# Kernel optimization log

Hardware: AMD Instinct MI355X
Metric: run time of the kernel (lower is better)

## Reference

```python
import jax, jax.numpy as jnp
import numpy as np

B, N, D = 8, 2048, 512  # batch, input_dim (tokens), weight_dim


def setup_inputs() -> dict:
    key = jax.random.key(0)
    ks = jax.random.split(key, 7)
    return {
        "query": jax.random.normal(ks[0], (B, N, D), dtype=jnp.float32),
        "key": jax.random.normal(ks[1], (B, N, D), dtype=jnp.float32),
        "value": jax.random.normal(ks[2], (B, N, D), dtype=jnp.float32),
        "W_query": jax.random.normal(ks[3], (D, D), dtype=jnp.float32),
        "W_key": jax.random.normal(ks[4], (D, D), dtype=jnp.float32),
        "W_value": jax.random.normal(ks[5], (D, D), dtype=jnp.float32),
        "self_importance": jnp.zeros((N,), dtype=jnp.float32),
    }


def reference(query, key, value, W_query, W_key, W_value, self_importance):
    d = W_query.shape[0]
    q = jnp.einsum("bnd,de->bne", query, W_query)
    k = jnp.einsum("bnd,de->bne", key, W_key)
    v = jnp.einsum("bnd,de->bne", value, W_value)
    scores = jnp.einsum("bqe,bke->bqk", q, k) / jnp.sqrt(jnp.float32(d))
    # diagonal self-importance bias: eye(N) * clamp(exp(s), max=3)
    importance = jnp.minimum(jnp.exp(self_importance), 3.0)  # [N]
    n = scores.shape[1]
    idx = jnp.arange(n)
    scores = scores.at[:, idx, idx].add(importance)
    attn = jax.nn.softmax(scores, axis=-1)  # [B, N, N]
    entropy_loss = -jnp.mean(jnp.sum(attn * jnp.log(attn + 1e-10), axis=-1))
    out = jnp.einsum("bqk,bke->bqe", attn, v)
    return (out, attn, entropy_loss)
```

## Files before the change

### kernel.cpp

```cpp
#include <hip/hip_runtime.h>
#include <math.h>

#define BB 8
#define NN 2048
#define DD 512

typedef _Float16 halfT;
typedef _Float16 half8 __attribute__((ext_vector_type(8)));
typedef _Float16 half4 __attribute__((ext_vector_type(4)));
typedef float f32x4 __attribute__((ext_vector_type(4)));

#define GLOAD16(gp, sp) __builtin_amdgcn_global_load_lds( \
    (const __attribute__((address_space(1))) void*)(gp), \
    (__attribute__((address_space(3))) void*)(sp), 16, 0, 0)

__global__ __launch_bounds__(256) void wsplit_kernel(
    const float* __restrict__ Wq, const float* __restrict__ Wk, const float* __restrict__ Wv,
    _Float16* __restrict__ qhT, _Float16* __restrict__ qlT,
    _Float16* __restrict__ khT, _Float16* __restrict__ klT,
    _Float16* __restrict__ vhT)
{
    __shared__ float t[64][65];
    const int z = blockIdx.z;
    const float* W = (z == 0) ? Wq : ((z == 1) ? Wk : Wv);
    _Float16* Ph = (z == 0) ? qhT : ((z == 1) ? khT : vhT);
    _Float16* Pl = (z == 0) ? qlT : ((z == 1) ? klT : nullptr);
    const int bx = blockIdx.x * 64, by = blockIdx.y * 64;
    const int tid = threadIdx.x;
    #pragma unroll
    for (int i = 0; i < 16; ++i) {
        const int idx = i * 256 + tid;
        const int r = idx >> 6, c = idx & 63;
        t[r][c] = W[(long)(by + r) * 512 + bx + c];
    }
    __syncthreads();
    #pragma unroll
    for (int i = 0; i < 16; ++i) {
        const int idx = i * 256 + tid;
        const int r = idx >> 6, c = idx & 63;
        const float v = t[c][r];
        const _Float16 h = (_Float16)v;
        const long o = (long)(bx + r) * 512 + by + c;
        Ph[o] = h;
        if (z < 2) Pl[o] = (_Float16)(v - (float)h);
    }
}

__global__ __launch_bounds__(256) void projqk_kernel(
    const float* __restrict__ Af0, const float* __restrict__ Af1,
    const _Float16* __restrict__ B0h, const _Float16* __restrict__ B0l,
    const _Float16* __restrict__ B1h, const _Float16* __restrict__ B1l,
    _Float16* __restrict__ O0h, _Float16* __restrict__ O0l,
    _Float16* __restrict__ O1h, _Float16* __restrict__ O1l)
{
    __shared__ __align__(16) _Float16 smem[4 * 128 * 32];
    _Float16* Ah = smem;
    _Float16* Bh = smem + 4096;
    _Float16* Al = smem + 8192;
    _Float16* Bl = smem + 12288;

    const int z = blockIdx.z;
    const float* Af = z ? Af1 : Af0;
    const _Float16* Bgh = z ? B1h : B0h;
    const _Float16* Bgl = z ? B1l : B0l;
    _Float16* Oh = z ? O1h : O0h;
    _Float16* Ol = z ? O1l : O0l;

    const int tid  = threadIdx.x;
    const int lane = tid & 63;
    const int w    = tid >> 6;
    const int wr   = w >> 1, wc = w & 1;
    const int bm   = blockIdx.y * 128, bn = blockIdx.x * 128;

    f32x4 acc[4][4];
    #pragma unroll
    for (int i = 0; i < 4; ++i)
        #pragma unroll
        for (int j = 0; j < 4; ++j) acc[i][j] = (f32x4)0.0f;

    for (int k0 = 0; k0 < DD; k0 += 32) {
        #pragma unroll
        for (int i = 0; i < 2; ++i) {
            const int c   = i * 256 + w * 64 + lane;
            const int row = c >> 2, sl = c & 3;
            const long g  = (long)(bn + row) * DD + k0 + sl * 8;
            const int lb  = (i * 256 + w * 64) * 8;
            GLOAD16(Bgh + g, Bh + lb);
            GLOAD16(Bgl + g, Bl + lb);
        }
        #pragma unroll
        for (int i = 0; i < 4; ++i) {
            const int c = tid + i * 256;
            const int row = c >> 3, q4 = c & 7;
            const float4 v = *(const float4*)(Af + (long)(bm + row) * DD + k0 + q4 * 4);
            half4 h;
            h[0] = (_Float16)v.x; h[1] = (_Float16)v.y;
            h[2] = (_Float16)v.z; h[3] = (_Float16)v.w;
            *(half4*)&Ah[row * 32 + q4 * 4] = h;
            half4 l;
            l[0] = (_Float16)(v.x - (float)h[0]);
            l[1] = (_Float16)(v.y - (float)h[1]);
            l[2] = (_Float16)(v.z - (float)h[2]);
            l[3] = (_Float16)(v.w - (float)h[3]);
            *(half4*)&Al[row * 32 + q4 * 4] = l;
        }
        __syncthreads();

        half8 ah[4], bh[4], al[4], bl[4];
        #pragma unroll
        for (int f = 0; f < 4; ++f) {
            const int ar = wr * 64 + f * 16 + (lane & 15);
            const int ao = ar * 32 + ((lane >> 4) << 3);
            ah[f] = *(const half8*)&Ah[ao];
            al[f] = *(const half8*)&Al[ao];
            const int br = wc * 64 + f * 16 + (lane & 15);
            const int bo = br * 32 + ((lane >> 4) << 3);
            bh[f] = *(const half8*)&Bh[bo];
            bl[f] = *(const half8*)&Bl[bo];
        }
        #pragma unroll
        for (int i = 0; i < 4; ++i)
            #pragma unroll
            for (int j = 0; j < 4; ++j) {
                acc[i][j] = __builtin_amdgcn_mfma_f32_16x16x32_f16(ah[i], bh[j], acc[i][j], 0, 0, 0);
                acc[i][j] = __builtin_amdgcn_mfma_f32_16x16x32_f16(ah[i], bl[j], acc[i][j], 0, 0, 0);
                acc[i][j] = __builtin_amdgcn_mfma_f32_16x16x32_f16(al[i], bh[j], acc[i][j], 0, 0, 0);
            }
        __syncthreads();
    }

    #pragma unroll
    for (int i = 0; i < 4; ++i) {
        const int rb = bm + wr * 64 + i * 16 + ((lane >> 4) << 2);
        #pragma unroll
        for (int j = 0; j < 4; ++j) {
            const int gc = bn + wc * 64 + j * 16 + (lane & 15);
            #pragma unroll
            for (int r = 0; r < 4; ++r) {
                const float vv = acc[i][j][r];
                const _Float16 h = (_Float16)vv;
                const long o = (long)(rb + r) * DD + gc;
                Oh[o] = h;
                Ol[o] = (_Float16)(vv - (float)h);
            }
        }
    }
}

template<int EPI>
__global__ __launch_bounds__(256) void mm_nt(
    const float* __restrict__ Af,
    const _Float16* __restrict__ Agh,
    const _Float16* __restrict__ Bgh,
    float* __restrict__ Of, _Float16* __restrict__ Oh,
    int N, int K, long sAb, long sBb, long sOb)
{
    constexpr bool A_FP32 = (EPI == 1);

    __shared__ __align__(16) _Float16 smem[2 * 128 * 32];
    _Float16* Ah = smem;
    _Float16* Bh = smem + 4096;

    const int tid  = threadIdx.x;
    const int lane = tid & 63;
    const int w    = tid >> 6;
    const int wr   = w >> 1, wc = w & 1;
    const int z    = blockIdx.z;
    const int bm   = blockIdx.y * 128, bn = blockIdx.x * 128;

    const float* Afz = nullptr;
    const _Float16* Aghz = nullptr;
    if constexpr (A_FP32) { Afz = Af + (long)z * sAb; }
    else { Aghz = Agh + (long)z * sAb; }
    const _Float16* Bghz = Bgh + (long)z * sBb;

    f32x4 acc[4][4];
    #pragma unroll
    for (int i = 0; i < 4; ++i)
        #pragma unroll
        for (int j = 0; j < 4; ++j) acc[i][j] = (f32x4)0.0f;

    for (int k0 = 0; k0 < K; k0 += 32) {
        #pragma unroll
        for (int i = 0; i < 2; ++i) {
            const int c   = i * 256 + w * 64 + lane;
            const int row = c >> 2, sl = c & 3;
            const long g  = (long)(bn + row) * K + k0 + sl * 8;
            const int lb  = (i * 256 + w * 64) * 8;
            GLOAD16(Bghz + g, Bh + lb);
        }
        if constexpr (A_FP32) {
            #pragma unroll
            for (int i = 0; i < 4; ++i) {
                const int c = tid + i * 256;
                const int row = c >> 3, q4 = c & 7;
                const float4 v = *(const float4*)(Afz + (long)(bm + row) * K + k0 + q4 * 4);
                half4 h;
                h[0] = (_Float16)v.x; h[1] = (_Float16)v.y;
                h[2] = (_Float16)v.z; h[3] = (_Float16)v.w;
                *(half4*)&Ah[row * 32 + q4 * 4] = h;
            }
        } else {
            #pragma unroll
            for (int i = 0; i < 2; ++i) {
                const int c   = i * 256 + w * 64 + lane;
                const int row = c >> 2, sl = c & 3;
                const long g  = (long)(bm + row) * K + k0 + sl * 8;
                const int lb  = (i * 256 + w * 64) * 8;
                GLOAD16(Aghz + g, Ah + lb);
            }
        }
        __syncthreads();

        half8 ah[4], bh[4];
        #pragma unroll
        for (int f = 0; f < 4; ++f) {
            const int ar = wr * 64 + f * 16 + (lane & 15);
            const int ao = ar * 32 + ((lane >> 4) << 3);
            ah[f] = *(const half8*)&Ah[ao];
            const int br = wc * 64 + f * 16 + (lane & 15);
            const int bo = br * 32 + ((lane >> 4) << 3);
            bh[f] = *(const half8*)&Bh[bo];
        }
        #pragma unroll
        for (int i = 0; i < 4; ++i)
            #pragma unroll
            for (int j = 0; j < 4; ++j)
                acc[i][j] = __builtin_amdgcn_mfma_f32_16x16x32_f16(ah[i], bh[j], acc[i][j], 0, 0, 0);
        __syncthreads();
    }

    #pragma unroll
    for (int i = 0; i < 4; ++i) {
        const int rb = bm + wr * 64 + i * 16 + ((lane >> 4) << 2);
        #pragma unroll
        for (int j = 0; j < 4; ++j) {
            const int gc = bn + wc * 64 + j * 16 + (lane & 15);
            if constexpr (EPI == 1) {
                half4 hv;
                #pragma unroll
                for (int r = 0; r < 4; ++r) hv[r] = (_Float16)acc[i][j][r];
                const int b = rb >> 11, rIn = rb & 2047;
                *(half4*)&Oh[((long)b * 512 + gc) * 2048 + rIn] = hv;
            } else {
                float* O = Of + (long)z * sOb;
                #pragma unroll
                for (int r = 0; r < 4; ++r)
                    O[(long)(rb + r) * N + gc] = acc[i][j][r];
            }
        }
    }
}

__global__ __launch_bounds__(512, 2) void scores256_kernel(
    const halfT* __restrict__ qh, const halfT* __restrict__ ql,
    const halfT* __restrict__ kh, const halfT* __restrict__ kl,
    float* __restrict__ C, const float* __restrict__ si, float scale)
{
    extern __shared__ __align__(16) char smem[];

    const int tid  = threadIdx.x;
    const int lane = tid & 63;
    const int w    = tid >> 6;
    const int wr   = w >> 2, wc = w & 3;

    int flat = (blockIdx.z << 6) | (blockIdx.y << 3) | blockIdx.x;
    flat = ((flat & 7) << 6) | (flat >> 3);
    const int bx = flat & 7, by = (flat >> 3) & 7, bz = flat >> 6;
    const int bm = by * 256, bn = bx * 256;

    const long zoff = (long)bz * NN * DD;
    const halfT* A_h = qh + zoff;
    const halfT* A_l = ql + zoff;
    const halfT* B_h = kh + zoff;
    const halfT* B_l = kl + zoff;

    const int s_row   = w * 16 + (lane >> 2);
    const int s_chunk = (lane & 3) ^ ((lane >> 3) & 3);
    const long gA = (long)(bm + s_row) * DD + s_chunk * 8;
    const long gB = (long)(bn + s_row) * DD + s_chunk * 8;
    const int ldst = w * 1024;
    const long rstep = (long)128 * DD;

    const int lr   = lane & 15;
    const int q16  = lane >> 4;
    const int frag = lr * 64 + ((q16 ^ ((lr >> 1) & 3)) << 4);
    const int abase = wr * 8192 + frag;
    const int bbase = wc * 4096 + frag;

    f32x4 acc[8][4];
    #pragma unroll
    for (int m = 0; m < 8; ++m)
        #pragma unroll
        for (int n = 0; n < 4; ++n) acc[m][n] = (f32x4)0.0f;

    {
        char* b0 = smem;
        GLOAD16(A_h + gA,         b0 + ldst);
        GLOAD16(A_h + gA + rstep, b0 + 8192 + ldst);
        GLOAD16(A_l + gA,         b0 + 16384 + ldst);
        GLOAD16(A_l + gA + rstep, b0 + 16384 + 8192 + ldst);
        GLOAD16(B_h + gB,         b0 + 32768 + ldst);
        GLOAD16(B_h + gB + rstep, b0 + 32768 + 8192 + ldst);
        GLOAD16(B_l + gB,         b0 + 49152 + ldst);
        GLOAD16(B_l + gB + rstep, b0 + 49152 + 8192 + ldst);
    }
    asm volatile("s_waitcnt vmcnt(0)" ::: "memory");
    __builtin_amdgcn_s_barrier();
    __builtin_amdgcn_sched_barrier(0);

    for (int t = 0; t < 16; ++t) {
        char* cur = smem + (size_t)(t & 1) * 65536;
        char* nxt = smem + (size_t)((t + 1) & 1) * 65536;
        const bool pf = (t < 15);
        const long kk = (long)(t + 1) * 32;

        half8 ah[8], bh[4];
        #pragma unroll
        for (int n = 0; n < 4; ++n)
            bh[n] = *(const half8*)(cur + 32768 + bbase + n * 1024);
        #pragma unroll
        for (int m = 0; m < 8; ++m)
            ah[m] = *(const half8*)(cur + abase + m * 1024);
        if (pf) {
            GLOAD16(A_h + gA + kk,         nxt + ldst);
            GLOAD16(A_h + gA + rstep + kk, nxt + 8192 + ldst);
            GLOAD16(A_l + gA + kk,         nxt + 16384 + ldst);
            GLOAD16(A_l + gA + rstep + kk, nxt + 16384 + 8192 + ldst);
        }
        __builtin_amdgcn_s_barrier();
        asm volatile("s_waitcnt lgkmcnt(0)" ::: "memory");
        __builtin_amdgcn_sched_barrier(0);
        __builtin_amdgcn_s_setprio(1);
        #pragma unroll
        for (int m = 0; m < 8; ++m)
            #pragma unroll
            for (int n = 0; n < 4; ++n)
                acc[m][n] = __builtin_amdgcn_mfma_f32_16x16x32_f16(ah[m], bh[n], acc[m][n], 0, 0, 0);
        __builtin_amdgcn_s_setprio(0);
        __builtin_amdgcn_s_barrier();
        __builtin_amdgcn_sched_barrier(0);

        half8 bl[4];
        #pragma unroll
        for (int n = 0; n < 4; ++n)
            bl[n] = *(const half8*)(cur + 49152 + bbase + n * 1024);
        if (pf) {
            GLOAD16(B_h + gB + kk,         nxt + 32768 + ldst);
            GLOAD16(B_h + gB + rstep + kk, nxt + 32768 + 8192 + ldst);
            GLOAD16(B_l + gB + kk,         nxt + 49152 + ldst);
            GLOAD16(B_l + gB + rstep + kk, nxt + 49152 + 8192 + ldst);
        }
        __builtin_amdgcn_s_barrier();
        asm volatile("s_waitcnt lgkmcnt(0)" ::: "memory");
        __builtin_amdgcn_sched_barrier(0);
        __builtin_amdgcn_s_setprio(1);
        #pragma unroll
        for (int m = 0; m < 8; ++m)
            #pragma unroll
            for (int n = 0; n < 4; ++n)
                acc[m][n] = __builtin_amdgcn_mfma_f32_16x16x32_f16(ah[m], bl[n], acc[m][n], 0, 0, 0);
        __builtin_amdgcn_s_setprio(0);
        __builtin_amdgcn_s_barrier();
        __builtin_amdgcn_sched_barrier(0);

        half8 al[8];
        #pragma unroll
        for (int m = 0; m < 8; ++m)
            al[m] = *(const half8*)(cur + 16384 + abase + m * 1024);
        __builtin_amdgcn_s_barrier();
        asm volatile("s_waitcnt lgkmcnt(0)" ::: "memory");
        __builtin_amdgcn_sched_barrier(0);
        __builtin_amdgcn_s_setprio(1);
        #pragma unroll
        for (int m = 0; m < 8; ++m)
            #pragma unroll
            for (int n = 0; n < 4; ++n)
                acc[m][n] = __builtin_amdgcn_mfma_f32_16x16x32_f16(al[m], bh[n], acc[m][n], 0, 0, 0);
        __builtin_amdgcn_s_setprio(0);
        if (pf) { asm volatile("s_waitcnt vmcnt(0)" ::: "memory"); }
        __builtin_amdgcn_s_barrier();
        __builtin_amdgcn_sched_barrier(0);
    }

    float* Cz = C + (long)bz * NN * NN;
    #pragma unroll
    for (int m = 0; m < 8; ++m) {
        const int rb = bm + wr * 128 + m * 16 + ((lane >> 4) << 2);
        #pragma unroll
        for (int n = 0; n < 4; ++n) {
            const int gc = bn + wc * 64 + n * 16 + (lane & 15);
            #pragma unroll
            for (int r = 0; r < 4; ++r) {
                const int gr = rb + r;
                float vv = acc[m][n][r] * scale;
                if (gr == gc) vv += fminf(expf(si[gr]), 3.0f);
                Cz[(long)gr * NN + gc] = vv;
            }
        }
    }
}

__global__ __launch_bounds__(256) void softmax_entropy_kernel(
    float* __restrict__ attn, _Float16* __restrict__ ah, float* __restrict__ partials)
{
    __shared__ float red[4];
    const long row = blockIdx.x;
    float* p = attn + row * (long)NN;
    _Float16* ph = ah + row * (long)NN;
    const int tid = threadIdx.x;
    const int base = tid * 8;

    float4 va = *(const float4*)(p + base);
    float4 vb = *(const float4*)(p + base + 4);
    float v[8] = {va.x, va.y, va.z, va.w, vb.x, vb.y, vb.z, vb.w};

    float m = v[0];
    #pragma unroll
    for (int i = 1; i < 8; ++i) m = fmaxf(m, v[i]);
    #pragma unroll
    for (int o = 32; o; o >>= 1) m = fmaxf(m, __shfl_xor(m, o, 64));
    if ((tid & 63) == 0) red[tid >> 6] = m;
    __syncthreads();
    m = fmaxf(fmaxf(red[0], red[1]), fmaxf(red[2], red[3]));

    float t[8];
    float s = 0.f;
    #pragma unroll
    for (int i = 0; i < 8; ++i) { t[i] = v[i] - m; v[i] = expf(t[i]); s += v[i]; }
    #pragma unroll
    for (int o = 32; o; o >>= 1) s += __shfl_xor(s, o, 64);
    __syncthreads();
    if ((tid & 63) == 0) red[tid >> 6] = s;
    __syncthreads();
    s = red[0] + red[1] + red[2] + red[3];

    const float inv = 1.0f / s;
    const float lns = logf(s);
    float e = 0.f;
    float pv[8];
    #pragma unroll
    for (int i = 0; i < 8; ++i) {
        pv[i] = v[i] * inv;
        e = fmaf(pv[i], t[i] - lns, e);
    }
    *(float4*)(p + base)     = make_float4(pv[0], pv[1], pv[2], pv[3]);
    *(float4*)(p + base + 4) = make_float4(pv[4], pv[5], pv[6], pv[7]);
    half8 h;
    #pragma unroll
    for (int i = 0; i < 8; ++i) h[i] = (_Float16)pv[i];
    *(half8*)(ph + base) = h;

    #pragma unroll
    for (int o = 32; o; o >>= 1) e += __shfl_xor(e, o, 64);
    __syncthreads();
    if ((tid & 63) == 0) red[tid >> 6] = e;
    __syncthreads();
    if (tid == 0) partials[row] = red[0] + red[1] + red[2] + red[3];
}

__global__ __launch_bounds__(256) void ent_reduce_kernel(
    const float* __restrict__ partials, float* __restrict__ ent)
{
    __shared__ float red[4];
    float s = 0.f;
    for (int i = threadIdx.x; i < BB * NN; i += 256) s += partials[i];
    #pragma unroll
    for (int o = 32; o; o >>= 1) s += __shfl_xor(s, o, 64);
    if ((threadIdx.x & 63) == 0) red[threadIdx.x >> 6] = s;
    __syncthreads();
    if (threadIdx.x == 0)
        *ent = -(red[0] + red[1] + red[2] + red[3]) / (float)(BB * NN);
}

extern "C" void kernel_launch(void* const* d_in, const int* in_sizes, int n_in,
                              void* d_out, int out_size, void* d_ws, size_t ws_size,
                              hipStream_t stream) {
    const float* query = (const float*)d_in[0];
    const float* key   = (const float*)d_in[1];
    const float* value = (const float*)d_in[2];
    const float* Wq    = (const float*)d_in[3];
    const float* Wk    = (const float*)d_in[4];
    const float* Wv    = (const float*)d_in[5];
    const float* si    = (const float*)d_in[6];

    float* out  = (float*)d_out;
    float* attn = out + (size_t)BB * NN * DD;
    float* ent  = attn + (size_t)BB * NN * NN;

    const size_t NK = (size_t)BB * NN * DD;
    _Float16* ws16 = (_Float16*)d_ws;
    _Float16* qh = ws16;
    _Float16* ql = qh + NK;
    _Float16* kh = ql + NK;
    _Float16* kl = kh + NK;
    _Float16* vT = kl + NK;
    _Float16* WqhT = vT + NK;
    _Float16* WqlT = WqhT + DD * DD;
    _Float16* WkhT = WqlT + DD * DD;
    _Float16* WklT = WkhT + DD * DD;
    _Float16* WvhT = WklT + DD * DD;
    float* partials = (float*)(WvhT + DD * DD);
    _Float16* attn_h = ws16;

    const dim3 blk(256);
    const float inv_sqrt_d = 0.044194173824159216f;

    wsplit_kernel<<<dim3(8, 8, 3), blk, 0, stream>>>(Wq, Wk, Wv,
        WqhT, WqlT, WkhT, WklT, WvhT);

    projqk_kernel<<<dim3(4, 128, 2), blk, 0, stream>>>(
        query, key, WqhT, WqlT, WkhT, WklT, qh, ql, kh, kl);
    mm_nt<1><<<dim3(4, 128, 1), blk, 0, stream>>>(
        value, nullptr, WvhT, nullptr, vT, DD, DD, 0, 0, 0);

    scores256_kernel<<<dim3(8, 8, 8), dim3(512), 131072, stream>>>(
        qh, ql, kh, kl, attn, si, inv_sqrt_d);

    softmax_entropy_kernel<<<dim3(BB * NN), blk, 0, stream>>>(attn, attn_h, partials);
    ent_reduce_kernel<<<dim3(1), blk, 0, stream>>>(partials, ent);

    mm_nt<3><<<dim3(4, 16, BB), blk, 0, stream>>>(
        nullptr, attn_h, vT, out, nullptr, DD, NN,
        (long)NN * NN, (long)DD * NN, (long)NN * DD);
}
```

Before: 335.7 us.

## Switch scores GEMM to 32x32 MFMA and add pipelined attn-V kernel

The scores kernel now uses 32x32x16 f16 MFMA tiles, which cuts LDS fragment reads per FLOP. It also issues the whole next-stage prefetch up front and drops the intermediate barriers, keeping one wait-and-barrier per k-step. The attn·V product moves from the generic 128x128 mm_nt to a new 256x128, 512-thread kernel with double-buffered LDS, direct-to-LDS loads, swizzled fragments and 32x32 MFMA. The V projection becomes a dedicated non-template kernel. The gain is higher MFMA throughput and better overlap. The costs are higher register pressure from the 16-wide accumulators and less fine-grained interleaving of loads with compute.

Result: no change. 335.0 us (-0.2%).

```diff
diff --git a/kernel.cpp b/kernel.cpp
--- a/kernel.cpp
+++ b/kernel.cpp
@@ -9,6 +9,7 @@
 typedef _Float16 half8 __attribute__((ext_vector_type(8)));
 typedef _Float16 half4 __attribute__((ext_vector_type(4)));
 typedef float f32x4 __attribute__((ext_vector_type(4)));
+typedef float f32x16 __attribute__((ext_vector_type(16)));
 
 #define GLOAD16(gp, sp) __builtin_amdgcn_global_load_lds( \
     (const __attribute__((address_space(1))) void*)(gp), \
@@ -147,16 +148,10 @@
     }
 }
 
-template<int EPI>
-__global__ __launch_bounds__(256) void mm_nt(
-    const float* __restrict__ Af,
-    const _Float16* __restrict__ Agh,
-    const _Float16* __restrict__ Bgh,
-    float* __restrict__ Of, _Float16* __restrict__ Oh,
-    int N, int K, long sAb, long sBb, long sOb)
-{
-    constexpr bool A_FP32 = (EPI == 1);
-
+__global__ __launch_bounds__(256) void vproj_kernel(
+    const float* __restrict__ Af, const _Float16* __restrict__ Bgh,
+    _Float16* __restrict__ Oh)
+{
     __shared__ __align__(16) _Float16 smem[2 * 128 * 32];
     _Float16* Ah = smem;
     _Float16* Bh = smem + 4096;
@@ -165,50 +160,32 @@
     const int lane = tid & 63;
     const int w    = tid >> 6;
     const int wr   = w >> 1, wc = w & 1;
-    const int z    = blockIdx.z;
     const int bm   = blockIdx.y * 128, bn = blockIdx.x * 128;
 
-    const float* Afz = nullptr;
-    const _Float16* Aghz = nullptr;
-    if constexpr (A_FP32) { Afz = Af + (long)z * sAb; }
-    else { Aghz = Agh + (long)z * sAb; }
-    const _Float16* Bghz = Bgh + (long)z * sBb;
-
     f32x4 acc[4][4];
     #pragma unroll
     for (int i = 0; i < 4; ++i)
         #pragma unroll
         for (int j = 0; j < 4; ++j) acc[i][j] = (f32x4)0.0f;
 
-    for (int k0 = 0; k0 < K; k0 += 32) {
+    for (int k0 = 0; k0 < DD; k0 += 32) {
         #pragma unroll
         for (int i = 0; i < 2; ++i) {
             const int c   = i * 256 + w * 64 + lane;
             const int row = c >> 2, sl = c & 3;
-            const long g  = (long)(bn + row) * K + k0 + sl * 8;
+            const long g  = (long)(bn + row) * DD + k0 + sl * 8;
             const int lb  = (i * 256 + w * 64) * 8;
-            GLOAD16(Bghz + g, Bh + lb);
-        }
-        if constexpr (A_FP32) {
-            #pragma unroll
-            for (int i = 0; i < 4; ++i) {
-                const int c = tid + i * 256;
-                const int row = c >> 3, q4 = c & 7;
-                const float4 v = *(const float4*)(Afz + (long)(bm + row) * K + k0 + q4 * 4);
-                half4 h;
-                h[0] = (_Float16)v.x; h[1] = (_Float16)v.y;
-                h[2] = (_Float16)v.z; h[3] = (_Float16)v.w;
-                *(half4*)&Ah[row * 32 + q4 * 4] = h;
-            }
-        } else {
-            #pragma unroll
-            for (int i = 0; i < 2; ++i) {
-                const int c   = i * 256 + w * 64 + lane;
-                const int row = c >> 2, sl = c & 3;
-                const long g  = (long)(bm + row) * K + k0 + sl * 8;
-                const int lb  = (i * 256 + w * 64) * 8;
-                GLOAD16(Aghz + g, Ah + lb);
-            }
+            GLOAD16(Bgh + g, Bh + lb);
+        }
+        #pragma unroll
+        for (int i = 0; i < 4; ++i) {
+            const int c = tid + i * 256;
+            const int row = c >> 3, q4 = c & 7;
+            const float4 v = *(const float4*)(Af + (long)(bm + row) * DD + k0 + q4 * 4);
+            half4 h;
+            h[0] = (_Float16)v.x; h[1] = (_Float16)v.y;
+            h[2] = (_Float16)v.z; h[3] = (_Float16)v.w;
+            *(half4*)&Ah[row * 32 + q4 * 4] = h;
         }
         __syncthreads();
 
@@ -216,11 +193,9 @@
         #pragma unroll
         for (int f = 0; f < 4; ++f) {
             const int ar = wr * 64 + f * 16 + (lane & 15);
-            const int ao = ar * 32 + ((lane >> 4) << 3);
-            ah[f] = *(const half8*)&Ah[ao];
+            ah[f] = *(const half8*)&Ah[ar * 32 + ((lane >> 4) << 3)];
             const int br = wc * 64 + f * 16 + (lane & 15);
-            const int bo = br * 32 + ((lane >> 4) << 3);
-            bh[f] = *(const half8*)&Bh[bo];
+            bh[f] = *(const half8*)&Bh[br * 32 + ((lane >> 4) << 3)];
         }
         #pragma unroll
         for (int i = 0; i < 4; ++i)
@@ -236,18 +211,11 @@
         #pragma unroll
         for (int j = 0; j < 4; ++j) {
             const int gc = bn + wc * 64 + j * 16 + (lane & 15);
-            if constexpr (EPI == 1) {
-                half4 hv;
-                #pragma unroll
-                for (int r = 0; r < 4; ++r) hv[r] = (_Float16)acc[i][j][r];
-                const int b = rb >> 11, rIn = rb & 2047;
-                *(half4*)&Oh[((long)b * 512 + gc) * 2048 + rIn] = hv;
-            } else {
-                float* O = Of + (long)z * sOb;
-                #pragma unroll
-                for (int r = 0; r < 4; ++r)
-                    O[(long)(rb + r) * N + gc] = acc[i][j][r];
-            }
+            half4 hv;
+            #pragma unroll
+            for (int r = 0; r < 4; ++r) hv[r] = (_Float16)acc[i][j][r];
+            const int b = rb >> 11, rIn = rb & 2047;
+            *(half4*)&Oh[((long)b * 512 + gc) * 2048 + rIn] = hv;
         }
     }
 }
@@ -282,29 +250,28 @@
     const int ldst = w * 1024;
     const long rstep = (long)128 * DD;
 
-    const int lr   = lane & 15;
-    const int q16  = lane >> 4;
-    const int frag = lr * 64 + ((q16 ^ ((lr >> 1) & 3)) << 4);
-    const int abase = wr * 8192 + frag;
-    const int bbase = wc * 4096 + frag;
-
-    f32x4 acc[8][4];
-    #pragma unroll
-    for (int m = 0; m < 8; ++m)
-        #pragma unroll
-        for (int n = 0; n < 4; ++n) acc[m][n] = (f32x4)0.0f;
-
-    {
-        char* b0 = smem;
-        GLOAD16(A_h + gA,         b0 + ldst);
-        GLOAD16(A_h + gA + rstep, b0 + 8192 + ldst);
-        GLOAD16(A_l + gA,         b0 + 16384 + ldst);
-        GLOAD16(A_l + gA + rstep, b0 + 16384 + 8192 + ldst);
-        GLOAD16(B_h + gB,         b0 + 32768 + ldst);
-        GLOAD16(B_h + gB + rstep, b0 + 32768 + 8192 + ldst);
-        GLOAD16(B_l + gB,         b0 + 49152 + ldst);
-        GLOAD16(B_l + gB + rstep, b0 + 49152 + 8192 + ldst);
-    }
+    auto stage = [&](char* buf, int t) {
+        const long kk = (long)t * 32;
+        GLOAD16(A_h + gA + kk,         buf + ldst);
+        GLOAD16(A_h + gA + rstep + kk, buf + 8192 + ldst);
+        GLOAD16(A_l + gA + kk,         buf + 16384 + ldst);
+        GLOAD16(A_l + gA + rstep + kk, buf + 16384 + 8192 + ldst);
+        GLOAD16(B_h + gB + kk,         buf + 32768 + ldst);
+        GLOAD16(B_h + gB + rstep + kk, buf + 32768 + 8192 + ldst);
+        GLOAD16(B_l + gB + kk,         buf + 49152 + ldst);
+        GLOAD16(B_l + gB + rstep + kk, buf + 49152 + 8192 + ldst);
+    };
+
+    const int frow = lane & 31;
+    const int fgr  = lane >> 5;
+
+    f32x16 acc[4][2];
+    #pragma unroll
+    for (int m = 0; m < 4; ++m)
+        #pragma unroll
+        for (int n = 0; n < 2; ++n) acc[m][n] = (f32x16)0.0f;
+
+    stage(smem, 0);
     asm volatile("s_waitcnt vmcnt(0)" ::: "memory");
     __builtin_amdgcn_s_barrier();
     __builtin_amdgcn_sched_barrier(0);
@@ -312,91 +279,176 @@
     for (int t = 0; t < 16; ++t) {
         char* cur = smem + (size_t)(t & 1) * 65536;
         char* nxt = smem + (size_t)((t + 1) & 1) * 65536;
-        const bool pf = (t < 15);
-        const long kk = (long)(t + 1) * 32;
-
-        half8 ah[8], bh[4];
-        #pragma unroll
-        for (int n = 0; n < 4; ++n)
-            bh[n] = *(const half8*)(cur + 32768 + bbase + n * 1024);
-        #pragma unroll
-        for (int m = 0; m < 8; ++m)
-            ah[m] = *(const half8*)(cur + abase + m * 1024);
-        if (pf) {
-            GLOAD16(A_h + gA + kk,         nxt + ldst);
-            GLOAD16(A_h + gA + rstep + kk, nxt + 8192 + ldst);
-            GLOAD16(A_l + gA + kk,         nxt + 16384 + ldst);
-            GLOAD16(A_l + gA + rstep + kk, nxt + 16384 + 8192 + ldst);
-        }
-        __builtin_amdgcn_s_barrier();
-        asm volatile("s_waitcnt lgkmcnt(0)" ::: "memory");
-        __builtin_amdgcn_sched_barrier(0);
+
+        if (t < 15) stage(nxt, t + 1);
+
+        auto fr = [&](const char* unit, int row, int kh) -> half8 {
+            const int g = kh * 2 + fgr;
+            const int phys = g ^ ((row >> 1) & 3);
+            return *(const half8*)(unit + row * 64 + phys * 16);
+        };
+
+        half8 a_[4][2], bh_[2][2];
+        #pragma unroll
+        for (int kh2 = 0; kh2 < 2; ++kh2) {
+            #pragma unroll
+            for (int n = 0; n < 2; ++n)
+                bh_[n][kh2] = fr(cur + 32768, wc * 64 + n * 32 + frow, kh2);
+            #pragma unroll
+            for (int m = 0; m < 4; ++m)
+                a_[m][kh2] = fr(cur, wr * 128 + m * 32 + frow, kh2);
+        }
         __builtin_amdgcn_s_setprio(1);
         #pragma unroll
-        for (int m = 0; m < 8; ++m)
-            #pragma unroll
-            for (int n = 0; n < 4; ++n)
-                acc[m][n] = __builtin_amdgcn_mfma_f32_16x16x32_f16(ah[m], bh[n], acc[m][n], 0, 0, 0);
+        for (int m = 0; m < 4; ++m)
+            #pragma unroll
+            for (int n = 0; n < 2; ++n)
+                #pragma unroll
+                for (int kh2 = 0; kh2 < 2; ++kh2)
+                    acc[m][n] = __builtin_amdgcn_mfma_f32_32x32x16_f16(a_[m][kh2], bh_[n][kh2], acc[m][n], 0, 0, 0);
         __builtin_amdgcn_s_setprio(0);
-        __builtin_amdgcn_s_barrier();
-        __builtin_amdgcn_sched_barrier(0);
-
-        half8 bl[4];
-        #pragma unroll
-        for (int n = 0; n < 4; ++n)
-            bl[n] = *(const half8*)(cur + 49152 + bbase + n * 1024);
-        if (pf) {
-            GLOAD16(B_h + gB + kk,         nxt + 32768 + ldst);
-            GLOAD16(B_h + gB + rstep + kk, nxt + 32768 + 8192 + ldst);
-            GLOAD16(B_l + gB + kk,         nxt + 49152 + ldst);
-            GLOAD16(B_l + gB + rstep + kk, nxt + 49152 + 8192 + ldst);
-        }
-        __builtin_amdgcn_s_barrier();
-        asm volatile("s_waitcnt lgkmcnt(0)" ::: "memory");
-        __builtin_amdgcn_sched_barrier(0);
+
+        half8 bl_[2][2];
+        #pragma unroll
+        for (int kh2 = 0; kh2 < 2; ++kh2)
+            #pragma unroll
+            for (int n = 0; n < 2; ++n)
+                bl_[n][kh2] = fr(cur + 49152, wc * 64 + n * 32 + frow, kh2);
         __builtin_amdgcn_s_setprio(1);
         #pragma unroll
-        for (int m = 0; m < 8; ++m)
-            #pragma unroll
-            for (int n = 0; n < 4; ++n)
-                acc[m][n] = __builtin_amdgcn_mfma_f32_16x16x32_f16(ah[m], bl[n], acc[m][n], 0, 0, 0);
+        for (int m = 0; m < 4; ++m)
+            #pragma unroll
+            for (int n = 0; n < 2; ++n)
+                #pragma unroll
+                for (int kh2 = 0; kh2 < 2; ++kh2)
+                    acc[m][n] = __builtin_amdgcn_mfma_f32_32x32x16_f16(a_[m][kh2], bl_[n][kh2], acc[m][n], 0, 0, 0);
         __builtin_amdgcn_s_setprio(0);
-        __builtin_amdgcn_s_barrier();
-        __builtin_amdgcn_sched_barrier(0);
-
-        half8 al[8];
-        #pragma unroll
-        for (int m = 0; m < 8; ++m)
-            al[m] = *(const half8*)(cur + 16384 + abase + m * 1024);
-        __builtin_amdgcn_s_barrier();
-        asm volatile("s_waitcnt lgkmcnt(0)" ::: "memory");
-        __builtin_amdgcn_sched_barrier(0);
+
         __builtin_amdgcn_s_setprio(1);
         #pragma unroll
-        for (int m = 0; m < 8; ++m)
-            #pragma unroll
-            for (int n = 0; n < 4; ++n)
-                acc[m][n] = __builtin_amdgcn_mfma_f32_16x16x32_f16(al[m], bh[n], acc[m][n], 0, 0, 0);
+        for (int m = 0; m < 4; ++m) {
+            half8 al0 = fr(cur + 16384, wr * 128 + m * 32 + frow, 0);
+            half8 al1 = fr(cur + 16384, wr * 128 + m * 32 + frow, 1);
+            #pragma unroll
+            for (int n = 0; n < 2; ++n) {
+                acc[m][n] = __builtin_amdgcn_mfma_f32_32x32x16_f16(al0, bh_[n][0], acc[m][n], 0, 0, 0);
+                acc[m][n] = __builtin_amdgcn_mfma_f32_32x32x16_f16(al1, bh_[n][1], acc[m][n], 0, 0, 0);
+            }
+        }
         __builtin_amdgcn_s_setprio(0);
-        if (pf) { asm volatile("s_waitcnt vmcnt(0)" ::: "memory"); }
-        __builtin_amdgcn_s_barrier();
-        __builtin_amdgcn_sched_barrier(0);
+
+        if (t < 15) {
+            asm volatile("s_waitcnt vmcnt(0)" ::: "memory");
+            __builtin_amdgcn_s_barrier();
+        }
     }
 
     float* Cz = C + (long)bz * NN * NN;
-    #pragma unroll
-    for (int m = 0; m < 8; ++m) {
-        const int rb = bm + wr * 128 + m * 16 + ((lane >> 4) << 2);
-        #pragma unroll
-        for (int n = 0; n < 4; ++n) {
-            const int gc = bn + wc * 64 + n * 16 + (lane & 15);
-            #pragma unroll
-            for (int r = 0; r < 4; ++r) {
-                const int gr = rb + r;
-                float vv = acc[m][n][r] * scale;
+    const int rbias = 4 * (lane >> 5);
+    #pragma unroll
+    for (int m = 0; m < 4; ++m) {
+        #pragma unroll
+        for (int n = 0; n < 2; ++n) {
+            const int gc = bn + wc * 64 + n * 32 + (lane & 31);
+            #pragma unroll
+            for (int reg = 0; reg < 16; ++reg) {
+                const int gr = bm + wr * 128 + m * 32 + (reg & 3) + 8 * (reg >> 2) + rbias;
+                float vv = acc[m][n][reg] * scale;
                 if (gr == gc) vv += fminf(expf(si[gr]), 3.0f);
                 Cz[(long)gr * NN + gc] = vv;
             }
+        }
+    }
+}
+
+__global__ __launch_bounds__(512, 2) void av_kernel(
+    const halfT* __restrict__ P, const halfT* __restrict__ V,
+    float* __restrict__ O)
+{
+    extern __shared__ __align__(16) char smem[];
+
+    const int tid  = threadIdx.x;
+    const int lane = tid & 63;
+    const int w    = tid >> 6;
+    const int wr   = w >> 2, wc = w & 3;
+
+    int flat = (blockIdx.z << 5) | (blockIdx.y << 2) | blockIdx.x;
+    flat = ((flat & 7) << 5) | (flat >> 3);
+    const int nx = flat & 3, my = (flat >> 2) & 7, bz = flat >> 5;
+    const int bm = my * 256, bn = nx * 128;
+
+    const halfT* A = P + (long)bz * NN * NN;
+    const halfT* B = V + (long)bz * DD * NN;
+
+    const int s_row   = w * 16 + (lane >> 2);
+    const int s_chunk = (lane & 3) ^ ((lane >> 3) & 3);
+    const long gA = (long)(bm + s_row) * NN + s_chunk * 8;
+    const long gB = (long)(bn + s_row) * NN + s_chunk * 8;
+    const int ldst = w * 1024;
+    const long rstep = (long)128 * NN;
+
+    auto stage = [&](char* buf, int t) {
+        const long kk = (long)t * 32;
+        GLOAD16(A + gA + kk,         buf + ldst);
+        GLOAD16(A + gA + rstep + kk, buf + 8192 + ldst);
+        GLOAD16(B + gB + kk,         buf + 16384 + ldst);
+    };
+
+    const int frow = lane & 31;
+    const int fgr  = lane >> 5;
+
+    f32x16 acc[4];
+    #pragma unroll
+    for (int m = 0; m < 4; ++m) acc[m] = (f32x16)0.0f;
+
+    stage(smem, 0);
+    asm volatile("s_waitcnt vmcnt(0)" ::: "memory");
+    __builtin_amdgcn_s_barrier();
+    __builtin_amdgcn_sched_barrier(0);
+
+    for (int t = 0; t < 64; ++t) {
+        char* cur = smem + (size_t)(t & 1) * 24576;
+        char* nxt = smem + (size_t)((t + 1) & 1) * 24576;
+
+        if (t < 63) stage(nxt, t + 1);
+
+        auto fr = [&](const char* unit, int row, int kh) -> half8 {
+            const int g = kh * 2 + fgr;
+            const int phys = g ^ ((row >> 1) & 3);
+            return *(const half8*)(unit + row * 64 + phys * 16);
+        };
+
+        half8 a_[4][2], b_[2];
+        #pragma unroll
+        for (int kh2 = 0; kh2 < 2; ++kh2) {
+            b_[kh2] = fr(cur + 16384, wc * 32 + frow, kh2);
+            #pragma unroll
+            for (int m = 0; m < 4; ++m)
+                a_[m][kh2] = fr(cur, wr * 128 + m * 32 + frow, kh2);
+        }
+        __builtin_amdgcn_s_setprio(1);
+        #pragma unroll
+        for (int m = 0; m < 4; ++m)
+            #pragma unroll
+            for (int kh2 = 0; kh2 < 2; ++kh2)
+                acc[m] = __builtin_amdgcn_mfma_f32_32x32x16_f16(a_[m][kh2], b_[kh2], acc[m], 0, 0, 0);
+        __builtin_amdgcn_s_setprio(0);
+
+        if (t < 63) {
+            asm volatile("s_waitcnt vmcnt(0)" ::: "memory");
+            __builtin_amdgcn_s_barrier();
+        }
+    }
+
+    float* Oz = O + (long)bz * NN * DD;
+    const int rbias = 4 * (lane >> 5);
+    const int gc = bn + wc * 32 + (lane & 31);
+    #pragma unroll
+    for (int m = 0; m < 4; ++m) {
+        #pragma unroll
+        for (int reg = 0; reg < 16; ++reg) {
+            const int gr = bm + wr * 128 + m * 32 + (reg & 3) + 8 * (reg >> 2) + rbias;
+            Oz[(long)gr * DD + gc] = acc[m][reg];
         }
     }
 }
@@ -511,8 +563,7 @@
 
     projqk_kernel<<<dim3(4, 128, 2), blk, 0, stream>>>(
         query, key, WqhT, WqlT, WkhT, WklT, qh, ql, kh, kl);
-    mm_nt<1><<<dim3(4, 128, 1), blk, 0, stream>>>(
-        value, nullptr, WvhT, nullptr, vT, DD, DD, 0, 0, 0);
+    vproj_kernel<<<dim3(4, 128, 1), blk, 0, stream>>>(value, WvhT, vT);
 
     scores256_kernel<<<dim3(8, 8, 8), dim3(512), 131072, stream>>>(
         qh, ql, kh, kl, attn, si, inv_sqrt_d);
@@ -520,7 +571,5 @@
     softmax_entropy_kernel<<<dim3(BB * NN), blk, 0, stream>>>(attn, attn_h, partials);
     ent_reduce_kernel<<<dim3(1), blk, 0, stream>>>(partials, ent);
 
-    mm_nt<3><<<dim3(4, 16, BB), blk, 0, stream>>>(
-        nullptr, attn_h, vT, out, nullptr, DD, NN,
-        (long)NN * NN, (long)DD * NN, (long)NN * DD);
-}
+    av_kernel<<<dim3(4, 8, 8), dim3(512), 49152, stream>>>(attn_h, vT, out);
+}
```
